# Optimization experiments

Hardware: AMD Instinct MI355X
Metric: run time of the kernel (lower is better)

The kernel has to match this reference:

```python
import jax, jax.numpy as jnp
import numpy as np

B, S, D, H = 4, 2048, 512, 8
HD = D // H  # head dim = 64


def setup_inputs() -> dict:
    key = jax.random.key(0)
    ks = jax.random.split(key, 7)
    s = 0.02
    return {
        "X": jax.random.normal(ks[0], (B, S, D), dtype=jnp.float32),
        "Y": jax.random.normal(ks[1], (B, S, D), dtype=jnp.float32),
        "Z": jax.random.normal(ks[2], (B, S, D), dtype=jnp.float32),
        # weights stored as [in, out] (torch Linear weight transposed)
        "Wq": jax.random.normal(ks[3], (D, D), dtype=jnp.float32) * s,
        "Wk": jax.random.normal(ks[4], (D, D), dtype=jnp.float32) * s,
        "Wv": jax.random.normal(ks[5], (D, D), dtype=jnp.float32) * s,  # dead in original forward
        "Wo": jax.random.normal(ks[6], (D, D), dtype=jnp.float32) * s,
    }


def _split_heads(t):
    # [B, S, D] -> [B, H, S, HD]
    return t.reshape(B, S, H, HD).transpose(0, 2, 1, 3)


def reference(X, Y, Z, Wq, Wk, Wv, Wo):
    q = _split_heads(X @ Wq)
    k = _split_heads(Y @ Wk)
    # NOTE: original module (faithfully) uses W_o for the value projection; W_v is unused.
    v = _split_heads(Z @ Wo)
    scores = jnp.einsum("bhqd,bhkd->bhqk", q, k) / jnp.sqrt(jnp.float32(HD))
    # sigmoid(s) > 0.5  <=>  s > 0 (sigmoid strictly monotone); keep score else 0
    scores = jnp.where(scores > 0, scores, jnp.float32(0))
    attn = jax.nn.softmax(scores, axis=-1)
    out = jnp.einsum("bhqk,bhkd->bhqd", attn, v)  # dropout inactive at eval
    out = out.transpose(0, 2, 1, 3).reshape(B, S, D)  # merge heads
    return out @ Wo
```

## Files before the change

kernel.cpp:

```cpp
#include <hip/hip_runtime.h>
#include <math.h>

#define S_LEN 2048
#define DIM   512
#define M_TOT 8192
#define NCH   (S_LEN / 64)

typedef __attribute__((ext_vector_type(8))) short bf16x8;
typedef __attribute__((ext_vector_type(4))) short bf16x4;
typedef __attribute__((ext_vector_type(4))) float f32x4;

#define MFMA(a, b, c) __builtin_amdgcn_mfma_f32_16x16x32_bf16((a), (b), (c), 0, 0, 0)

__device__ __forceinline__ short f2b(float x) {
    union { float f; unsigned u; } v; v.f = x;
    unsigned r = v.u + 0x7FFFu + ((v.u >> 16) & 1u);
    return (short)(r >> 16);
}

__global__ __launch_bounds__(256) void cvt_bf16(const float* __restrict__ X,
                                                const float* __restrict__ Y,
                                                const float* __restrict__ Z,
                                                short* __restrict__ Xb,
                                                short* __restrict__ Yb,
                                                short* __restrict__ Zb) {
    const int zi = blockIdx.y;
    const float* A = zi == 0 ? X : zi == 1 ? Y : Z;
    short* O = zi == 0 ? Xb : zi == 1 ? Yb : Zb;
    const size_t i = (size_t)blockIdx.x * 256 + threadIdx.x;
    float4 a = ((const float4*)A)[2 * i];
    float4 b = ((const float4*)A)[2 * i + 1];
    bf16x8 o = { f2b(a.x), f2b(a.y), f2b(a.z), f2b(a.w),
                 f2b(b.x), f2b(b.y), f2b(b.z), f2b(b.w) };
    *(bf16x8*)&O[i * 8] = o;
}

__global__ __launch_bounds__(256) void prep_wt(const float* Wq, const float* Wk, const float* Wo,
                                               short* Wtq, short* Wtk, short* Wto) {
    const int zi = blockIdx.z;
    const float* W = zi == 0 ? Wq : zi == 1 ? Wk : Wo;
    short*      Wt = zi == 0 ? Wtq : zi == 1 ? Wtk : Wto;
    __shared__ short Ts[64 * 72];
    const int t = threadIdx.x;
    const int k0 = blockIdx.x * 64, n0 = blockIdx.y * 64;
    #pragma unroll
    for (int it = 0; it < 4; ++it) {
        const int r = (t >> 4) + 16 * it;
        const int cq = t & 15;
        float4 v = *(const float4*)&W[(size_t)(k0 + r) * DIM + n0 + cq * 4];
        Ts[(4 * cq + 0) * 72 + r] = f2b(v.x);
        Ts[(4 * cq + 1) * 72 + r] = f2b(v.y);
        Ts[(4 * cq + 2) * 72 + r] = f2b(v.z);
        Ts[(4 * cq + 3) * 72 + r] = f2b(v.w);
    }
    __syncthreads();
    #pragma unroll
    for (int it = 0; it < 2; ++it) {
        const int n = (t >> 3) + 32 * it;
        const int sg = t & 7;
        *(bf16x8*)&Wt[(size_t)(n0 + n) * DIM + k0 + sg * 8] = *(const bf16x8*)&Ts[n * 72 + sg * 8];
    }
}

__global__ __launch_bounds__(256) void proj_gemm(const short* __restrict__ Xb,
                                                 const short* __restrict__ Yb,
                                                 const short* __restrict__ Zb,
                                                 const short* __restrict__ Wtq,
                                                 const short* __restrict__ Wtk,
                                                 const short* __restrict__ Wto,
                                                 short* __restrict__ Qb,
                                                 short* __restrict__ Kb,
                                                 short* __restrict__ Vt) {
    const int zi = blockIdx.z;
    const short* A  = zi == 0 ? Xb : zi == 1 ? Yb : Zb;
    const short* Bw = zi == 0 ? Wtq : zi == 1 ? Wtk : Wto;

    __shared__ short As[128 * 40];
    __shared__ short Bs[128 * 40];
    const int tid = threadIdx.x;
    const int w = tid >> 6, ln = tid & 63, l15 = ln & 15, quad = ln >> 4;
    const int m0 = blockIdx.x * 128, n0 = blockIdx.y * 128;
    const int wm = (w & 1) * 64, wn = (w >> 1) * 64;

    const int r0 = tid >> 2, r1 = r0 + 64;
    const int sg = tid & 3;
    const short* ap0 = A  + (size_t)(m0 + r0) * DIM + sg * 8;
    const short* ap1 = A  + (size_t)(m0 + r1) * DIM + sg * 8;
    const short* bp0 = Bw + (size_t)(n0 + r0) * DIM + sg * 8;
    const short* bp1 = Bw + (size_t)(n0 + r1) * DIM + sg * 8;

    bf16x8 a0 = *(const bf16x8*)ap0, a1 = *(const bf16x8*)ap1;
    bf16x8 b0 = *(const bf16x8*)bp0, b1 = *(const bf16x8*)bp1;

    f32x4 acc[4][4] = {};

    for (int k0 = 0; k0 < DIM; k0 += 32) {
        __syncthreads();
        *(bf16x8*)&As[r0 * 40 + sg * 8] = a0;
        *(bf16x8*)&As[r1 * 40 + sg * 8] = a1;
        *(bf16x8*)&Bs[r0 * 40 + sg * 8] = b0;
        *(bf16x8*)&Bs[r1 * 40 + sg * 8] = b1;
        __syncthreads();
        const int kn = (k0 + 32 < DIM) ? k0 + 32 : 0;
        a0 = *(const bf16x8*)(ap0 + kn); a1 = *(const bf16x8*)(ap1 + kn);
        b0 = *(const bf16x8*)(bp0 + kn); b1 = *(const bf16x8*)(bp1 + kn);

        bf16x8 af[4], bf[4];
        #pragma unroll
        for (int mf = 0; mf < 4; ++mf) af[mf] = *(const bf16x8*)&As[(wm + 16 * mf + l15) * 40 + quad * 8];
        #pragma unroll
        for (int nf = 0; nf < 4; ++nf) bf[nf] = *(const bf16x8*)&Bs[(wn + 16 * nf + l15) * 40 + quad * 8];
        #pragma unroll
        for (int mf = 0; mf < 4; ++mf)
            #pragma unroll
            for (int nf = 0; nf < 4; ++nf)
                acc[mf][nf] = MFMA(af[mf], bf[nf], acc[mf][nf]);
    }

    if (zi < 2) {
        short* C = zi == 0 ? Qb : Kb;
        #pragma unroll
        for (int mf = 0; mf < 4; ++mf)
            #pragma unroll
            for (int nf = 0; nf < 4; ++nf)
                #pragma unroll
                for (int r = 0; r < 4; ++r)
                    C[(size_t)(m0 + wm + 16 * mf + 4 * quad + r) * DIM + n0 + wn + 16 * nf + l15] =
                        f2b(acc[mf][nf][r]);
    } else {
        #pragma unroll
        for (int mf = 0; mf < 4; ++mf)
            #pragma unroll
            for (int nf = 0; nf < 4; ++nf) {
                const int col = n0 + wn + 16 * nf + l15;
                const int h = col >> 6, hd = col & 63;
                const int row0_ = m0 + wm + 16 * mf + 4 * quad;
                const int bb = row0_ >> 11, s0 = row0_ & 2047;
                bf16x4 o = { f2b(acc[mf][nf][0]), f2b(acc[mf][nf][1]),
                             f2b(acc[mf][nf][2]), f2b(acc[mf][nf][3]) };
                *(bf16x4*)&Vt[((size_t)((bb * 8 + h) * 64 + hd)) * S_LEN + s0] = o;
            }
    }
}

__global__ __launch_bounds__(256) void out_gemm(const short* __restrict__ Ob,
                                                const short* __restrict__ Wto,
                                                float* __restrict__ Cout) {
    __shared__ short As[128 * 40];
    __shared__ short Bs[128 * 40];
    const int tid = threadIdx.x;
    const int w = tid >> 6, ln = tid & 63, l15 = ln & 15, quad = ln >> 4;
    const int m0 = blockIdx.x * 128, n0 = blockIdx.y * 128;
    const int wm = (w & 1) * 64, wn = (w >> 1) * 64;

    const int r0 = tid >> 2, r1 = r0 + 64;
    const int sg = tid & 3;
    const short* ap0 = Ob  + (size_t)(m0 + r0) * DIM + sg * 8;
    const short* ap1 = Ob  + (size_t)(m0 + r1) * DIM + sg * 8;
    const short* bp0 = Wto + (size_t)(n0 + r0) * DIM + sg * 8;
    const short* bp1 = Wto + (size_t)(n0 + r1) * DIM + sg * 8;

    bf16x8 a0 = *(const bf16x8*)ap0, a1 = *(const bf16x8*)ap1;
    bf16x8 b0 = *(const bf16x8*)bp0, b1 = *(const bf16x8*)bp1;

    f32x4 acc[4][4] = {};

    for (int k0 = 0; k0 < DIM; k0 += 32) {
        __syncthreads();
        *(bf16x8*)&As[r0 * 40 + sg * 8] = a0;
        *(bf16x8*)&As[r1 * 40 + sg * 8] = a1;
        *(bf16x8*)&Bs[r0 * 40 + sg * 8] = b0;
        *(bf16x8*)&Bs[r1 * 40 + sg * 8] = b1;
        __syncthreads();
        const int kn = (k0 + 32 < DIM) ? k0 + 32 : 0;
        a0 = *(const bf16x8*)(ap0 + kn); a1 = *(const bf16x8*)(ap1 + kn);
        b0 = *(const bf16x8*)(bp0 + kn); b1 = *(const bf16x8*)(bp1 + kn);

        bf16x8 af[4], bf[4];
        #pragma unroll
        for (int mf = 0; mf < 4; ++mf) af[mf] = *(const bf16x8*)&As[(wm + 16 * mf + l15) * 40 + quad * 8];
        #pragma unroll
        for (int nf = 0; nf < 4; ++nf) bf[nf] = *(const bf16x8*)&Bs[(wn + 16 * nf + l15) * 40 + quad * 8];
        #pragma unroll
        for (int mf = 0; mf < 4; ++mf)
            #pragma unroll
            for (int nf = 0; nf < 4; ++nf)
                acc[mf][nf] = MFMA(af[mf], bf[nf], acc[mf][nf]);
    }
    #pragma unroll
    for (int mf = 0; mf < 4; ++mf)
        #pragma unroll
        for (int nf = 0; nf < 4; ++nf)
            #pragma unroll
            for (int r = 0; r < 4; ++r)
                Cout[(size_t)(m0 + wm + 16 * mf + 4 * quad + r) * DIM + n0 + wn + 16 * nf + l15] =
                    acc[mf][nf][r];
}

__global__ __launch_bounds__(256) void attn_mfma(const short* __restrict__ Qb,
                                                 const short* __restrict__ Kb,
                                                 const short* __restrict__ Vtg,
                                                 short* __restrict__ Ob) {
    __shared__ short Ks[2][64 * 72];
    __shared__ short Vs[2][64 * 72];
    __shared__ short Es[4][32 * 72];

    const int tid = threadIdx.x;
    const int w = tid >> 6, ln = tid & 63, l15 = ln & 15, quad = ln >> 4;
    const int qt0 = blockIdx.x * 128;
    const int bh = blockIdx.y, b = bh >> 3, h = bh & 7;
    const size_t tokbase = (size_t)b * S_LEN;

    bf16x8 qf[2][2];
    #pragma unroll
    for (int nf = 0; nf < 2; ++nf)
        #pragma unroll
        for (int ks = 0; ks < 2; ++ks)
            qf[nf][ks] = *(const bf16x8*)&Qb[(tokbase + qt0 + 32 * w + 16 * nf + l15) * DIM +
                                             h * 64 + 32 * ks + 8 * quad];

    const int srow = tid >> 3, ssg = tid & 7;
    const short* kbase = Kb  + (tokbase + srow) * DIM + h * 64 + ssg * 8;
    const short* vbase = Vtg + ((size_t)bh * 64 + srow) * S_LEN + ssg * 8;

    bf16x8 k0r, k1r, v0r, v1r;

    f32x4 oacc[2][4] = {};
    float dsum[2] = {0.f, 0.f};

    {
        k0r = *(const bf16x8*)kbase;
        k1r = *(const bf16x8*)(kbase + (size_t)32 * DIM);
        v0r = *(const bf16x8*)vbase;
        v1r = *(const bf16x8*)(vbase + (size_t)32 * S_LEN);
        *(bf16x8*)&Ks[0][srow * 72 + ssg * 8] = k0r;
        *(bf16x8*)&Ks[0][(srow + 32) * 72 + ssg * 8] = k1r;
        *(bf16x8*)&Vs[0][srow * 72 + ssg * 8] = v0r;
        *(bf16x8*)&Vs[0][(srow + 32) * 72 + ssg * 8] = v1r;
        k0r = *(const bf16x8*)(kbase + (size_t)64 * DIM);
        k1r = *(const bf16x8*)(kbase + (size_t)96 * DIM);
        v0r = *(const bf16x8*)(vbase + 64);
        v1r = *(const bf16x8*)(vbase + (size_t)32 * S_LEN + 64);
    }
    __syncthreads();

    for (int kc = 0; kc < NCH; ++kc) {
        const int cur = kc & 1;
        if (kc + 1 < NCH) {
            *(bf16x8*)&Ks[cur ^ 1][srow * 72 + ssg * 8] = k0r;
            *(bf16x8*)&Ks[cur ^ 1][(srow + 32) * 72 + ssg * 8] = k1r;
            *(bf16x8*)&Vs[cur ^ 1][srow * 72 + ssg * 8] = v0r;
            *(bf16x8*)&Vs[cur ^ 1][(srow + 32) * 72 + ssg * 8] = v1r;
        }
        if (kc + 2 < NCH) {
            const size_t ko = (size_t)(kc + 2) * 64 * DIM;
            const size_t vo = (size_t)(kc + 2) * 64;
            k0r = *(const bf16x8*)(kbase + ko);
            k1r = *(const bf16x8*)(kbase + ko + (size_t)32 * DIM);
            v0r = *(const bf16x8*)(vbase + vo);
            v1r = *(const bf16x8*)(vbase + vo + (size_t)32 * S_LEN);
        }

        f32x4 sacc[4][2];
        #pragma unroll
        for (int mf = 0; mf < 4; ++mf) {
            bf16x8 ka = *(const bf16x8*)&Ks[cur][(16 * mf + l15) * 72 + 8 * quad];
            bf16x8 kb = *(const bf16x8*)&Ks[cur][(16 * mf + l15) * 72 + 32 + 8 * quad];
            #pragma unroll
            for (int nf = 0; nf < 2; ++nf) {
                f32x4 s = {0.f, 0.f, 0.f, 0.f};
                s = MFMA(ka, qf[nf][0], s);
                s = MFMA(kb, qf[nf][1], s);
                sacc[mf][nf] = s;
            }
        }

        short* Esw = &Es[w][0];
        #pragma unroll
        for (int mf = 0; mf < 4; ++mf)
            #pragma unroll
            for (int nf = 0; nf < 2; ++nf) {
                bf16x4 e4;
                #pragma unroll
                for (int r = 0; r < 4; ++r) {
                    const float e = __expf(fmaxf(sacc[mf][nf][r], 0.f) * 0.125f);
                    dsum[nf] += e;
                    e4[r] = f2b(e);
                }
                *(bf16x4*)&Esw[(16 * nf + l15) * 72 + 16 * mf + 4 * quad] = e4;
            }

        bf16x8 e00 = *(const bf16x8*)&Esw[l15 * 72 + 8 * quad];
        bf16x8 e01 = *(const bf16x8*)&Esw[l15 * 72 + 32 + 8 * quad];
        bf16x8 e10 = *(const bf16x8*)&Esw[(16 + l15) * 72 + 8 * quad];
        bf16x8 e11 = *(const bf16x8*)&Esw[(16 + l15) * 72 + 32 + 8 * quad];
        #pragma unroll
        for (int nf2 = 0; nf2 < 4; ++nf2) {
            bf16x8 vf0 = *(const bf16x8*)&Vs[cur][(16 * nf2 + l15) * 72 + 8 * quad];
            bf16x8 vf1 = *(const bf16x8*)&Vs[cur][(16 * nf2 + l15) * 72 + 32 + 8 * quad];
            oacc[0][nf2] = MFMA(e00, vf0, oacc[0][nf2]);
            oacc[0][nf2] = MFMA(e01, vf1, oacc[0][nf2]);
            oacc[1][nf2] = MFMA(e10, vf0, oacc[1][nf2]);
            oacc[1][nf2] = MFMA(e11, vf1, oacc[1][nf2]);
        }
        __syncthreads();
    }

    #pragma unroll
    for (int nf = 0; nf < 2; ++nf) {
        dsum[nf] += __shfl_xor(dsum[nf], 16);
        dsum[nf] += __shfl_xor(dsum[nf], 32);
    }
    const float dinv0 = 1.0f / dsum[0];
    const float dinv1 = 1.0f / dsum[1];

    #pragma unroll
    for (int mf2 = 0; mf2 < 2; ++mf2) {
        const float dv = mf2 ? dinv1 : dinv0;
        #pragma unroll
        for (int r = 0; r < 4; ++r) {
            const float di = __shfl(dv, 4 * quad + r);
            const size_t rowaddr = (tokbase + qt0 + 32 * w + 16 * mf2 + 4 * quad + r) * DIM + h * 64;
            #pragma unroll
            for (int nf2 = 0; nf2 < 4; ++nf2)
                Ob[rowaddr + 16 * nf2 + l15] = f2b(oacc[mf2][nf2][r] * di);
        }
    }
}

extern "C" void kernel_launch(void* const* d_in, const int* in_sizes, int n_in,
                              void* d_out, int out_size, void* d_ws, size_t ws_size,
                              hipStream_t stream) {
    const float* X  = (const float*)d_in[0];
    const float* Y  = (const float*)d_in[1];
    const float* Z  = (const float*)d_in[2];
    const float* Wq = (const float*)d_in[3];
    const float* Wk = (const float*)d_in[4];
    const float* Wo = (const float*)d_in[6];

    char* p = (char*)d_ws;
    const size_t MD = (size_t)M_TOT * DIM;
    short* Qb  = (short*)p; p += MD * 2;
    short* Kb  = (short*)p; p += MD * 2;
    short* Vt  = (short*)p; p += MD * 2;
    short* Ob  = (short*)p; p += MD * 2;
    short* Xb  = (short*)p; p += MD * 2;
    short* Yb  = (short*)p; p += MD * 2;
    short* Zb  = (short*)p; p += MD * 2;
    short* Wtq = (short*)p; p += (size_t)DIM * DIM * 2;
    short* Wtk = (short*)p; p += (size_t)DIM * DIM * 2;
    short* Wto = (short*)p; p += (size_t)DIM * DIM * 2;

    cvt_bf16<<<dim3(M_TOT * DIM / 8 / 256, 3), 256, 0, stream>>>(X, Y, Z, Xb, Yb, Zb);
    prep_wt<<<dim3(8, 8, 3), 256, 0, stream>>>(Wq, Wk, Wo, Wtq, Wtk, Wto);
    proj_gemm<<<dim3(64, 4, 3), 256, 0, stream>>>(Xb, Yb, Zb, Wtq, Wtk, Wto, Qb, Kb, Vt);
    attn_mfma<<<dim3(16, 32), 256, 0, stream>>>(Qb, Kb, Vt, Ob);
    out_gemm<<<dim3(64, 4), 256, 0, stream>>>(Ob, Wto, (float*)d_out);
}
```

Baseline: 215.8 us.

## Fuse fp32-to-bf16 input conversion into projection GEMM and streamline attention softmax

```diff
diff --git a/kernel.cpp b/kernel.cpp
--- a/kernel.cpp
+++ b/kernel.cpp
@@ -12,27 +12,35 @@
 
 #define MFMA(a, b, c) __builtin_amdgcn_mfma_f32_16x16x32_bf16((a), (b), (c), 0, 0, 0)
 
+#define QSCALE 0.18033688011112042f
+
 __device__ __forceinline__ short f2b(float x) {
     union { float f; unsigned u; } v; v.f = x;
     unsigned r = v.u + 0x7FFFu + ((v.u >> 16) & 1u);
     return (short)(r >> 16);
 }
 
-__global__ __launch_bounds__(256) void cvt_bf16(const float* __restrict__ X,
-                                                const float* __restrict__ Y,
-                                                const float* __restrict__ Z,
-                                                short* __restrict__ Xb,
-                                                short* __restrict__ Yb,
-                                                short* __restrict__ Zb) {
-    const int zi = blockIdx.y;
-    const float* A = zi == 0 ? X : zi == 1 ? Y : Z;
-    short* O = zi == 0 ? Xb : zi == 1 ? Yb : Zb;
-    const size_t i = (size_t)blockIdx.x * 256 + threadIdx.x;
-    float4 a = ((const float4*)A)[2 * i];
-    float4 b = ((const float4*)A)[2 * i + 1];
-    bf16x8 o = { f2b(a.x), f2b(a.y), f2b(a.z), f2b(a.w),
-                 f2b(b.x), f2b(b.y), f2b(b.z), f2b(b.w) };
-    *(bf16x8*)&O[i * 8] = o;
+__device__ __forceinline__ unsigned cvtpk(float a, float b) {
+    unsigned r;
+    asm("v_cvt_pk_bf16_f32 %0, %1, %2" : "=v"(r) : "v"(a), "v"(b));
+    return r;
+}
+
+__device__ __forceinline__ bf16x8 cvt8(float4 lo, float4 hi) {
+    union { unsigned u[4]; bf16x8 v; } o;
+    o.u[0] = cvtpk(lo.x, lo.y);
+    o.u[1] = cvtpk(lo.z, lo.w);
+    o.u[2] = cvtpk(hi.x, hi.y);
+    o.u[3] = cvtpk(hi.z, hi.w);
+    return o.v;
+}
+
+__device__ __forceinline__ float fast_exp2(float x) {
+#if __has_builtin(__builtin_amdgcn_exp2f)
+    return __builtin_amdgcn_exp2f(x);
+#else
+    return __expf(x * 0.693147180559945f);
+#endif
 }
 
 __global__ __launch_bounds__(256) void prep_wt(const float* Wq, const float* Wk, const float* Wo,
@@ -40,6 +48,7 @@
     const int zi = blockIdx.z;
     const float* W = zi == 0 ? Wq : zi == 1 ? Wk : Wo;
     short*      Wt = zi == 0 ? Wtq : zi == 1 ? Wtk : Wto;
+    const float sc = zi == 0 ? QSCALE : 1.0f;
     __shared__ short Ts[64 * 72];
     const int t = threadIdx.x;
     const int k0 = blockIdx.x * 64, n0 = blockIdx.y * 64;
@@ -48,10 +57,10 @@
         const int r = (t >> 4) + 16 * it;
         const int cq = t & 15;
         float4 v = *(const float4*)&W[(size_t)(k0 + r) * DIM + n0 + cq * 4];
-        Ts[(4 * cq + 0) * 72 + r] = f2b(v.x);
-        Ts[(4 * cq + 1) * 72 + r] = f2b(v.y);
-        Ts[(4 * cq + 2) * 72 + r] = f2b(v.z);
-        Ts[(4 * cq + 3) * 72 + r] = f2b(v.w);
+        Ts[(4 * cq + 0) * 72 + r] = f2b(v.x * sc);
+        Ts[(4 * cq + 1) * 72 + r] = f2b(v.y * sc);
+        Ts[(4 * cq + 2) * 72 + r] = f2b(v.z * sc);
+        Ts[(4 * cq + 3) * 72 + r] = f2b(v.w * sc);
     }
     __syncthreads();
     #pragma unroll
@@ -62,9 +71,9 @@
     }
 }
 
-__global__ __launch_bounds__(256) void proj_gemm(const short* __restrict__ Xb,
-                                                 const short* __restrict__ Yb,
-                                                 const short* __restrict__ Zb,
+__global__ __launch_bounds__(256) void proj_gemm(const float* __restrict__ X,
+                                                 const float* __restrict__ Y,
+                                                 const float* __restrict__ Z,
                                                  const short* __restrict__ Wtq,
                                                  const short* __restrict__ Wtk,
                                                  const short* __restrict__ Wto,
@@ -72,7 +81,7 @@
                                                  short* __restrict__ Kb,
                                                  short* __restrict__ Vt) {
     const int zi = blockIdx.z;
-    const short* A  = zi == 0 ? Xb : zi == 1 ? Yb : Zb;
+    const float* A  = zi == 0 ? X : zi == 1 ? Y : Z;
     const short* Bw = zi == 0 ? Wtq : zi == 1 ? Wtk : Wto;
 
     __shared__ short As[128 * 40];
@@ -84,25 +93,27 @@
 
     const int r0 = tid >> 2, r1 = r0 + 64;
     const int sg = tid & 3;
-    const short* ap0 = A  + (size_t)(m0 + r0) * DIM + sg * 8;
-    const short* ap1 = A  + (size_t)(m0 + r1) * DIM + sg * 8;
+    const float* ap0 = A  + (size_t)(m0 + r0) * DIM + sg * 8;
+    const float* ap1 = A  + (size_t)(m0 + r1) * DIM + sg * 8;
     const short* bp0 = Bw + (size_t)(n0 + r0) * DIM + sg * 8;
     const short* bp1 = Bw + (size_t)(n0 + r1) * DIM + sg * 8;
 
-    bf16x8 a0 = *(const bf16x8*)ap0, a1 = *(const bf16x8*)ap1;
+    float4 a0l = *(const float4*)ap0, a0h = *(const float4*)(ap0 + 4);
+    float4 a1l = *(const float4*)ap1, a1h = *(const float4*)(ap1 + 4);
     bf16x8 b0 = *(const bf16x8*)bp0, b1 = *(const bf16x8*)bp1;
 
     f32x4 acc[4][4] = {};
 
     for (int k0 = 0; k0 < DIM; k0 += 32) {
         __syncthreads();
-        *(bf16x8*)&As[r0 * 40 + sg * 8] = a0;
-        *(bf16x8*)&As[r1 * 40 + sg * 8] = a1;
+        *(bf16x8*)&As[r0 * 40 + sg * 8] = cvt8(a0l, a0h);
+        *(bf16x8*)&As[r1 * 40 + sg * 8] = cvt8(a1l, a1h);
         *(bf16x8*)&Bs[r0 * 40 + sg * 8] = b0;
         *(bf16x8*)&Bs[r1 * 40 + sg * 8] = b1;
         __syncthreads();
         const int kn = (k0 + 32 < DIM) ? k0 + 32 : 0;
-        a0 = *(const bf16x8*)(ap0 + kn); a1 = *(const bf16x8*)(ap1 + kn);
+        a0l = *(const float4*)(ap0 + kn); a0h = *(const float4*)(ap0 + kn + 4);
+        a1l = *(const float4*)(ap1 + kn); a1h = *(const float4*)(ap1 + kn + 4);
         b0 = *(const bf16x8*)(bp0 + kn); b1 = *(const bf16x8*)(bp1 + kn);
 
         bf16x8 af[4], bf[4];
@@ -207,8 +218,12 @@
 
     const int tid = threadIdx.x;
     const int w = tid >> 6, ln = tid & 63, l15 = ln & 15, quad = ln >> 4;
-    const int qt0 = blockIdx.x * 128;
-    const int bh = blockIdx.y, b = bh >> 3, h = bh & 7;
+
+    const int lin = blockIdx.y * 16 + blockIdx.x;
+    const int swz = ((lin & 7) << 6) + (lin >> 3);
+    const int qt0 = (swz & 15) * 128;
+    const int bh  = swz >> 4;
+    const int b = bh >> 3, h = bh & 7;
     const size_t tokbase = (size_t)b * S_LEN;
 
     bf16x8 qf[2][2];
@@ -226,7 +241,7 @@
     bf16x8 k0r, k1r, v0r, v1r;
 
     f32x4 oacc[2][4] = {};
-    float dsum[2] = {0.f, 0.f};
+    f32x4 d4[2] = {};
 
     {
         k0r = *(const bf16x8*)kbase;
@@ -262,6 +277,7 @@
         }
 
         f32x4 sacc[4][2];
+        __builtin_amdgcn_s_setprio(1);
         #pragma unroll
         for (int mf = 0; mf < 4; ++mf) {
             bf16x8 ka = *(const bf16x8*)&Ks[cur][(16 * mf + l15) * 72 + 8 * quad];
@@ -274,26 +290,30 @@
                 sacc[mf][nf] = s;
             }
         }
+        __builtin_amdgcn_s_setprio(0);
 
         short* Esw = &Es[w][0];
         #pragma unroll
         for (int mf = 0; mf < 4; ++mf)
             #pragma unroll
             for (int nf = 0; nf < 2; ++nf) {
-                bf16x4 e4;
-                #pragma unroll
-                for (int r = 0; r < 4; ++r) {
-                    const float e = __expf(fmaxf(sacc[mf][nf][r], 0.f) * 0.125f);
-                    dsum[nf] += e;
-                    e4[r] = f2b(e);
-                }
-                *(bf16x4*)&Esw[(16 * nf + l15) * 72 + 16 * mf + 4 * quad] = e4;
+                const float e0 = fast_exp2(fmaxf(sacc[mf][nf][0], 0.f));
+                const float e1 = fast_exp2(fmaxf(sacc[mf][nf][1], 0.f));
+                const float e2 = fast_exp2(fmaxf(sacc[mf][nf][2], 0.f));
+                const float e3 = fast_exp2(fmaxf(sacc[mf][nf][3], 0.f));
+                d4[nf][0] += e0; d4[nf][1] += e1;
+                d4[nf][2] += e2; d4[nf][3] += e3;
+                uint2 p;
+                p.x = cvtpk(e0, e1);
+                p.y = cvtpk(e2, e3);
+                *(uint2*)&Esw[(16 * nf + l15) * 72 + 16 * mf + 4 * quad] = p;
             }
 
         bf16x8 e00 = *(const bf16x8*)&Esw[l15 * 72 + 8 * quad];
         bf16x8 e01 = *(const bf16x8*)&Esw[l15 * 72 + 32 + 8 * quad];
         bf16x8 e10 = *(const bf16x8*)&Esw[(16 + l15) * 72 + 8 * quad];
         bf16x8 e11 = *(const bf16x8*)&Esw[(16 + l15) * 72 + 32 + 8 * quad];
+        __builtin_amdgcn_s_setprio(1);
         #pragma unroll
         for (int nf2 = 0; nf2 < 4; ++nf2) {
             bf16x8 vf0 = *(const bf16x8*)&Vs[cur][(16 * nf2 + l15) * 72 + 8 * quad];
@@ -303,11 +323,14 @@
             oacc[1][nf2] = MFMA(e10, vf0, oacc[1][nf2]);
             oacc[1][nf2] = MFMA(e11, vf1, oacc[1][nf2]);
         }
-        __syncthreads();
-    }
-
+        __builtin_amdgcn_s_setprio(0);
+        __syncthreads();
+    }
+
+    float dsum[2];
     #pragma unroll
     for (int nf = 0; nf < 2; ++nf) {
+        dsum[nf] = (d4[nf][0] + d4[nf][1]) + (d4[nf][2] + d4[nf][3]);
         dsum[nf] += __shfl_xor(dsum[nf], 16);
         dsum[nf] += __shfl_xor(dsum[nf], 32);
     }
@@ -344,16 +367,12 @@
     short* Kb  = (short*)p; p += MD * 2;
     short* Vt  = (short*)p; p += MD * 2;
     short* Ob  = (short*)p; p += MD * 2;
-    short* Xb  = (short*)p; p += MD * 2;
-    short* Yb  = (short*)p; p += MD * 2;
-    short* Zb  = (short*)p; p += MD * 2;
     short* Wtq = (short*)p; p += (size_t)DIM * DIM * 2;
     short* Wtk = (short*)p; p += (size_t)DIM * DIM * 2;
     short* Wto = (short*)p; p += (size_t)DIM * DIM * 2;
 
-    cvt_bf16<<<dim3(M_TOT * DIM / 8 / 256, 3), 256, 0, stream>>>(X, Y, Z, Xb, Yb, Zb);
     prep_wt<<<dim3(8, 8, 3), 256, 0, stream>>>(Wq, Wk, Wo, Wtq, Wtk, Wto);
-    proj_gemm<<<dim3(64, 4, 3), 256, 0, stream>>>(Xb, Yb, Zb, Wtq, Wtk, Wto, Qb, Kb, Vt);
+    proj_gemm<<<dim3(64, 4, 3), 256, 0, stream>>>(X, Y, Z, Wtq, Wtk, Wto, Qb, Kb, Vt);
     attn_mfma<<<dim3(16, 32), 256, 0, stream>>>(Qb, Kb, Vt, Ob);
     out_gemm<<<dim3(64, 4), 256, 0, stream>>>(Ob, Wto, (float*)d_out);
 }
```

Result: faster. 208.7 us (-3.3%).
